# Performance work log

Hardware: AMD Instinct MI355X
Metric: run time of the kernel (lower is better)

Reference implementation:

```python
import jax, jax.numpy as jnp
import numpy as np


def _rpad(x):
    # reflect-pad by 1 on both sides along the last dim (matches torch helper)
    return jnp.concatenate([x[..., 1:2], x, x[..., -2:-1]], axis=-1)


def _fwd1d(x):
    # LeGall 5/3 forward lifting along the last dim
    even = x[..., 0::2]
    odd = x[..., 1::2]
    e = _rpad(even)
    pred = 0.5 * (e[..., :-2] + e[..., 2:])
    d = odd - pred                      # detail
    de = _rpad(d)
    upd = 0.25 * (de[..., :-2] + de[..., 2:])
    s = even + upd                      # approx
    return s, d


def setup_inputs() -> dict:
    key = jax.random.key(0)
    # (B, C, H, W) with even H, W so the odd-size reflect pad branch is inactive
    x = jax.random.normal(key, (8, 3, 1024, 1024), dtype=jnp.float32)
    return {"x": x}


def reference(x):
    # rows: transform along W (last dim)
    s_row, d_row = _fwd1d(x)
    # columns: transform along H by swapping H<->W, lifting, swapping back
    LL, LH = _fwd1d(jnp.swapaxes(s_row, 2, 3))
    HL, HH = _fwd1d(jnp.swapaxes(d_row, 2, 3))
    LL, LH, HL, HH = (jnp.swapaxes(t, 2, 3) for t in (LL, LH, HL, HH))
    # (B, 4C, H/2, W/2) subband order [LL, LH, HL, HH]
    return jnp.concatenate([LL, LH, HL, HH], axis=1)
```

## Files before the change

kernel.cpp:

```cpp
#include <hip/hip_runtime.h>


static __device__ __forceinline__ int mref(int k) {
    return k < 0 ? 1 : (k > 511 ? 510 : k);
}

static __device__ __forceinline__ float4 lift_sub(float4 o, float4 em, float4 ep) {
    float4 r;
    r.x = o.x - 0.5f * (em.x + ep.x);
    r.y = o.y - 0.5f * (em.y + ep.y);
    r.z = o.z - 0.5f * (em.z + ep.z);
    r.w = o.w - 0.5f * (em.w + ep.w);
    return r;
}

static __device__ __forceinline__ float4 lift_add(float4 e, float4 dm, float4 dp) {
    float4 r;
    r.x = e.x + 0.25f * (dm.x + dp.x);
    r.y = e.y + 0.25f * (dm.y + dp.y);
    r.z = e.z + 0.25f * (dm.z + dp.z);
    r.w = e.w + 0.25f * (dm.w + dp.w);
    return r;
}

__global__ __launch_bounds__(256) void ilwt53_v4(const float* __restrict__ x,
                                                 float* __restrict__ out) {
    const int tid = threadIdx.x;
    const int c0  = blockIdx.x * 32;
    const int r0  = blockIdx.y * 32;
    const int img = blockIdx.z;
    const int rb  = 2 * r0 - 4;

    __shared__ float sS[71 * 36];
    __shared__ float sD[71 * 36];

    const float* __restrict__ xim = x + (size_t)img * (1024 * 1024);

    #pragma unroll
    for (int it = 0; it < 2; ++it) {
        int i = tid + it * 256;
        if (i < 284) {
            int lr = i >> 2, g = i & 3;
            int gy = rb + lr; gy = gy < 0 ? 0 : (gy > 1023 ? 1023 : gy);
            const float* __restrict__ row = xim + (size_t)gy * 1024;
            int c  = c0 + 8 * g;
            int fb = 2 * c - 4;

            float w[24];
            if (fb >= 0 && fb + 23 <= 1023) {
                const float4* p = (const float4*)(row + fb);
                #pragma unroll
                for (int q = 0; q < 6; ++q) {
                    float4 v = p[q];
                    w[4*q] = v.x; w[4*q+1] = v.y; w[4*q+2] = v.z; w[4*q+3] = v.w;
                }
            } else {
                #pragma unroll
                for (int q = 0; q < 24; ++q) {
                    int gx = fb + q; gx = gx < 0 ? 0 : (gx > 1023 ? 1023 : gx);
                    w[q] = row[gx];
                }
            }
            float d[10];
            #pragma unroll
            for (int t = 0; t < 10; ++t)
                d[t] = w[2*t+3] - 0.5f * (w[2*t] + w[2*t+4]);
            if (c == 0)   d[1] = w[5]  - w[6];
            if (c == 504) d[8] = w[19] - w[16];

            float s[8];
            #pragma unroll
            for (int i2 = 0; i2 < 8; ++i2)
                s[i2] = w[2*i2+4] + 0.25f * (d[i2] + d[i2+2]);
            if (c == 0)   s[0] = w[4]  + 0.5f * d[2];
            if (c == 504) s[7] = w[18] + 0.5f * d[7];

            float4* ps = (float4*)(sS + lr * 36 + 8 * g);
            ps[0] = make_float4(s[0], s[1], s[2], s[3]);
            ps[1] = make_float4(s[4], s[5], s[6], s[7]);
            float4* pd = (float4*)(sD + lr * 36 + 8 * g);
            pd[0] = make_float4(d[1], d[2], d[3], d[4]);
            pd[1] = make_float4(d[5], d[6], d[7], d[8]);
        }
    }
    __syncthreads();

    {
        const int rr = tid >> 3, ccg = tid & 7;
        const int r  = r0 + rr;
        const int co = 4 * ccg;
        const int k1 = mref(r - 1), k2 = mref(r + 1);
        const int ka = mref(k1 - 1), kb = mref(k1 + 1);
        const int kc = mref(k2 - 1), kd = mref(k2 + 1);

        #define SE_(k) (*(const float4*)(sS + (2 * ((k) - r0) + 4) * 36 + co))
        #define SO_(k) (*(const float4*)(sS + (2 * ((k) - r0) + 5) * 36 + co))
        #define DE_(k) (*(const float4*)(sD + (2 * ((k) - r0) + 4) * 36 + co))
        #define DO_(k) (*(const float4*)(sD + (2 * ((k) - r0) + 5) * 36 + co))

        const size_t plane = 512 * 512;
        float* __restrict__ ob = out + ((size_t)(img / 3) * 12 + (img % 3)) * plane;
        const size_t o = (size_t)r * 512 + c0 + co;

        {
            float4 se_r  = SE_(r);
            float4 se_k1 = SE_(k1);
            float4 se_k2 = SE_(k2);
            float4 se_a  = SE_(ka);
            float4 se_b  = SE_(kb);
            float4 se_c  = SE_(kc);
            float4 se_d  = SE_(kd);
            float4 so_r  = SO_(r);
            float4 so_k1 = SO_(k1);
            float4 so_k2 = SO_(k2);

            float4 lh_c = lift_sub(so_r,  se_k1, se_k2);
            float4 lh_m = lift_sub(so_k1, se_a,  se_b);
            float4 lh_p = lift_sub(so_k2, se_c,  se_d);
            float4 ll   = lift_add(se_r, lh_m, lh_p);

            *(float4*)(ob + o)             = ll;
            *(float4*)(ob + o + 3 * plane) = lh_c;
        }
        {
            float4 de_r  = DE_(r);
            float4 de_k1 = DE_(k1);
            float4 de_k2 = DE_(k2);
            float4 de_a  = DE_(ka);
            float4 de_b  = DE_(kb);
            float4 de_c  = DE_(kc);
            float4 de_d  = DE_(kd);
            float4 do_r  = DO_(r);
            float4 do_k1 = DO_(k1);
            float4 do_k2 = DO_(k2);

            float4 hh_c = lift_sub(do_r,  de_k1, de_k2);
            float4 hh_m = lift_sub(do_k1, de_a,  de_b);
            float4 hh_p = lift_sub(do_k2, de_c,  de_d);
            float4 hl   = lift_add(de_r, hh_m, hh_p);

            *(float4*)(ob + o + 6 * plane) = hl;
            *(float4*)(ob + o + 9 * plane) = hh_c;
        }
        #undef SE_
        #undef SO_
        #undef DE_
        #undef DO_
    }
}

extern "C" void kernel_launch(void* const* d_in, const int* in_sizes, int n_in,
                              void* d_out, int out_size, void* d_ws, size_t ws_size,
                              hipStream_t stream) {
    const float* x = (const float*)d_in[0];
    float* out = (float*)d_out;
    dim3 grid(16, 16, 24);
    dim3 block(256);
    hipLaunchKernelGGL(ilwt53_v4, grid, block, 0, stream, x, out);
}
```

Measured before the change: 178.3 us.

## Drop shared-memory staging and recompute row lifts per thread from global loads

Each thread now performs the horizontal lifting for the eight input rows it needs directly from global memory and computes its output column-lift in registers. The shared-memory tile and the block barrier are removed. The aim is to cut LDS traffic, synchronisation and the halo-staging phase. In exchange, each input row is loaded and lifted by several threads (about 4x redundant loads and ALU work), so the kernel leans on L1/L2 caching to absorb the repeated reads.

```diff
diff --git a/kernel.cpp b/kernel.cpp
--- a/kernel.cpp
+++ b/kernel.cpp
@@ -23,130 +23,86 @@
     return r;
 }
 
-__global__ __launch_bounds__(256) void ilwt53_v4(const float* __restrict__ x,
+static __device__ __forceinline__ void hlift4(const float* __restrict__ row,
+                                              int c, float4* s4, float4* d4) {
+    const int fb = 2 * c - 4;
+    float w[16];
+    if (fb >= 0 && fb + 15 <= 1023) {
+        const float4* p = (const float4*)(row + fb);
+        #pragma unroll
+        for (int q = 0; q < 4; ++q) {
+            float4 v = p[q];
+            w[4*q+0] = v.x; w[4*q+1] = v.y; w[4*q+2] = v.z; w[4*q+3] = v.w;
+        }
+    } else {
+        #pragma unroll
+        for (int t = 0; t < 16; ++t) {
+            int gx = fb + t; gx = gx < 0 ? 0 : (gx > 1023 ? 1023 : gx);
+            w[t] = row[gx];
+        }
+    }
+    float dd[6];
+    #pragma unroll
+    for (int t = 0; t < 6; ++t)
+        dd[t] = w[2*t+3] - 0.5f * (w[2*t] + w[2*t+4]);
+    if (c == 0)   { dd[1] = w[5]  - w[6]; dd[0] = dd[2]; }
+    if (c == 508) { dd[4] = w[11] - w[8]; dd[5] = dd[3]; }
+    float ss[4];
+    #pragma unroll
+    for (int i = 0; i < 4; ++i)
+        ss[i] = w[2*i+4] + 0.25f * (dd[i] + dd[i+2]);
+    *s4 = make_float4(ss[0], ss[1], ss[2], ss[3]);
+    *d4 = make_float4(dd[1], dd[2], dd[3], dd[4]);
+}
+
+__global__ __launch_bounds__(256) void ilwt53_v5(const float* __restrict__ x,
                                                  float* __restrict__ out) {
     const int tid = threadIdx.x;
     const int c0  = blockIdx.x * 32;
     const int r0  = blockIdx.y * 32;
     const int img = blockIdx.z;
-    const int rb  = 2 * r0 - 4;
-
-    __shared__ float sS[71 * 36];
-    __shared__ float sD[71 * 36];
 
     const float* __restrict__ xim = x + (size_t)img * (1024 * 1024);
 
-    #pragma unroll
-    for (int it = 0; it < 2; ++it) {
-        int i = tid + it * 256;
-        if (i < 284) {
-            int lr = i >> 2, g = i & 3;
-            int gy = rb + lr; gy = gy < 0 ? 0 : (gy > 1023 ? 1023 : gy);
-            const float* __restrict__ row = xim + (size_t)gy * 1024;
-            int c  = c0 + 8 * g;
-            int fb = 2 * c - 4;
+    const int rr = tid >> 3, ccg = tid & 7;
+    const int r  = r0 + rr;
+    const int c  = c0 + 4 * ccg;
 
-            float w[24];
-            if (fb >= 0 && fb + 23 <= 1023) {
-                const float4* p = (const float4*)(row + fb);
-                #pragma unroll
-                for (int q = 0; q < 6; ++q) {
-                    float4 v = p[q];
-                    w[4*q] = v.x; w[4*q+1] = v.y; w[4*q+2] = v.z; w[4*q+3] = v.w;
-                }
-            } else {
-                #pragma unroll
-                for (int q = 0; q < 24; ++q) {
-                    int gx = fb + q; gx = gx < 0 ? 0 : (gx > 1023 ? 1023 : gx);
-                    w[q] = row[gx];
-                }
-            }
-            float d[10];
-            #pragma unroll
-            for (int t = 0; t < 10; ++t)
-                d[t] = w[2*t+3] - 0.5f * (w[2*t] + w[2*t+4]);
-            if (c == 0)   d[1] = w[5]  - w[6];
-            if (c == 504) d[8] = w[19] - w[16];
+    const int k1 = mref(r - 1), k2 = mref(r + 1);
+    const int ka = mref(k1 - 1), kd = mref(k2 + 1);
 
-            float s[8];
-            #pragma unroll
-            for (int i2 = 0; i2 < 8; ++i2)
-                s[i2] = w[2*i2+4] + 0.25f * (d[i2] + d[i2+2]);
-            if (c == 0)   s[0] = w[4]  + 0.5f * d[2];
-            if (c == 504) s[7] = w[18] + 0.5f * d[7];
+    float4 se_a, de_a, se_1, de_1, se_r, de_r, se_2, de_2, se_d, de_d;
+    float4 so_1, do_1, so_r, do_r, so_2, do_2;
+    hlift4(xim + (size_t)(2 * ka)     * 1024, c, &se_a, &de_a);
+    hlift4(xim + (size_t)(2 * k1)     * 1024, c, &se_1, &de_1);
+    hlift4(xim + (size_t)(2 * r )     * 1024, c, &se_r, &de_r);
+    hlift4(xim + (size_t)(2 * k2)     * 1024, c, &se_2, &de_2);
+    hlift4(xim + (size_t)(2 * kd)     * 1024, c, &se_d, &de_d);
+    hlift4(xim + (size_t)(2 * k1 + 1) * 1024, c, &so_1, &do_1);
+    hlift4(xim + (size_t)(2 * r  + 1) * 1024, c, &so_r, &do_r);
+    hlift4(xim + (size_t)(2 * k2 + 1) * 1024, c, &so_2, &do_2);
 
-            float4* ps = (float4*)(sS + lr * 36 + 8 * g);
-            ps[0] = make_float4(s[0], s[1], s[2], s[3]);
-            ps[1] = make_float4(s[4], s[5], s[6], s[7]);
-            float4* pd = (float4*)(sD + lr * 36 + 8 * g);
-            pd[0] = make_float4(d[1], d[2], d[3], d[4]);
-            pd[1] = make_float4(d[5], d[6], d[7], d[8]);
-        }
-    }
-    __syncthreads();
+    const float4 seB = (r == 0)   ? se_d : se_r;
+    const float4 seE = (r == 511) ? se_a : se_r;
+    const float4 deB = (r == 0)   ? de_d : de_r;
+    const float4 deE = (r == 511) ? de_a : de_r;
 
-    {
-        const int rr = tid >> 3, ccg = tid & 7;
-        const int r  = r0 + rr;
-        const int co = 4 * ccg;
-        const int k1 = mref(r - 1), k2 = mref(r + 1);
-        const int ka = mref(k1 - 1), kb = mref(k1 + 1);
-        const int kc = mref(k2 - 1), kd = mref(k2 + 1);
+    const float4 lh_m = lift_sub(so_1, se_a, seB);
+    const float4 lh_c = lift_sub(so_r, se_1, se_2);
+    const float4 lh_p = lift_sub(so_2, seE, se_d);
+    const float4 ll   = lift_add(se_r, lh_m, lh_p);
+    const float4 hh_m = lift_sub(do_1, de_a, deB);
+    const float4 hh_c = lift_sub(do_r, de_1, de_2);
+    const float4 hh_p = lift_sub(do_2, deE, de_d);
+    const float4 hl   = lift_add(de_r, hh_m, hh_p);
 
-        #define SE_(k) (*(const float4*)(sS + (2 * ((k) - r0) + 4) * 36 + co))
-        #define SO_(k) (*(const float4*)(sS + (2 * ((k) - r0) + 5) * 36 + co))
-        #define DE_(k) (*(const float4*)(sD + (2 * ((k) - r0) + 4) * 36 + co))
-        #define DO_(k) (*(const float4*)(sD + (2 * ((k) - r0) + 5) * 36 + co))
-
-        const size_t plane = 512 * 512;
-        float* __restrict__ ob = out + ((size_t)(img / 3) * 12 + (img % 3)) * plane;
-        const size_t o = (size_t)r * 512 + c0 + co;
-
-        {
-            float4 se_r  = SE_(r);
-            float4 se_k1 = SE_(k1);
-            float4 se_k2 = SE_(k2);
-            float4 se_a  = SE_(ka);
-            float4 se_b  = SE_(kb);
-            float4 se_c  = SE_(kc);
-            float4 se_d  = SE_(kd);
-            float4 so_r  = SO_(r);
-            float4 so_k1 = SO_(k1);
-            float4 so_k2 = SO_(k2);
-
-            float4 lh_c = lift_sub(so_r,  se_k1, se_k2);
-            float4 lh_m = lift_sub(so_k1, se_a,  se_b);
-            float4 lh_p = lift_sub(so_k2, se_c,  se_d);
-            float4 ll   = lift_add(se_r, lh_m, lh_p);
-
-            *(float4*)(ob + o)             = ll;
-            *(float4*)(ob + o + 3 * plane) = lh_c;
-        }
-        {
-            float4 de_r  = DE_(r);
-            float4 de_k1 = DE_(k1);
-            float4 de_k2 = DE_(k2);
-            float4 de_a  = DE_(ka);
-            float4 de_b  = DE_(kb);
-            float4 de_c  = DE_(kc);
-            float4 de_d  = DE_(kd);
-            float4 do_r  = DO_(r);
-            float4 do_k1 = DO_(k1);
-            float4 do_k2 = DO_(k2);
-
-            float4 hh_c = lift_sub(do_r,  de_k1, de_k2);
-            float4 hh_m = lift_sub(do_k1, de_a,  de_b);
-            float4 hh_p = lift_sub(do_k2, de_c,  de_d);
-            float4 hl   = lift_add(de_r, hh_m, hh_p);
-
-            *(float4*)(ob + o + 6 * plane) = hl;
-            *(float4*)(ob + o + 9 * plane) = hh_c;
-        }
-        #undef SE_
-        #undef SO_
-        #undef DE_
-        #undef DO_
-    }
+    const size_t plane = 512 * 512;
+    float* __restrict__ ob = out + ((size_t)(img / 3) * 12 + (img % 3)) * plane;
+    const size_t o = (size_t)r * 512 + c;
+    *(float4*)(ob + o)             = ll;
+    *(float4*)(ob + o + 3 * plane) = lh_c;
+    *(float4*)(ob + o + 6 * plane) = hl;
+    *(float4*)(ob + o + 9 * plane) = hh_c;
 }
 
 extern "C" void kernel_launch(void* const* d_in, const int* in_sizes, int n_in,
@@ -156,5 +112,5 @@
     float* out = (float*)d_out;
     dim3 grid(16, 16, 24);
     dim3 block(256);
-    hipLaunchKernelGGL(ilwt53_v4, grid, block, 0, stream, x, out);
+    hipLaunchKernelGGL(ilwt53_v5, grid, block, 0, stream, x, out);
 }
```

Result: slower. 209.1 us (+17.3%).

## Stage raw input tile in shared memory with coalesced float4 loads

Applied to the files above, without the earlier changes.

Adds a first phase where all threads cooperatively load the 71x72 raw input halo tile into shared memory using contiguous float4 loads issued in batch. The row-lifting phase then reads its 24-wide windows from LDS instead of doing strided per-thread global loads. The S and D buffers are merged into one interleaved array with an odd float4 row stride to reduce bank conflicts. This costs an extra barrier and more LDS per block, which may lower occupancy.

```diff
diff --git a/kernel.cpp b/kernel.cpp
--- a/kernel.cpp
+++ b/kernel.cpp
@@ -23,7 +23,9 @@
     return r;
 }
 
-__global__ __launch_bounds__(256) void ilwt53_v4(const float* __restrict__ x,
+#define RSTRIDE 19
+
+__global__ __launch_bounds__(256) void ilwt53_v6(const float* __restrict__ x,
                                                  float* __restrict__ out) {
     const int tid = threadIdx.x;
     const int c0  = blockIdx.x * 32;
@@ -31,43 +33,64 @@
     const int img = blockIdx.z;
     const int rb  = 2 * r0 - 4;
 
-    __shared__ float sS[71 * 36];
-    __shared__ float sD[71 * 36];
+    __shared__ float4 raw4[71 * RSTRIDE];
+    __shared__ float4 sd4 [71 * RSTRIDE];
 
     const float* __restrict__ xim = x + (size_t)img * (1024 * 1024);
+
+    {
+        float4 v[5];
+        int    dst[5];
+        bool   act[5];
+        #pragma unroll
+        for (int it = 0; it < 5; ++it) {
+            int idx = tid + it * 256;
+            act[it] = idx < 71 * 18;
+            if (act[it]) {
+                int rw = idx / 18;
+                int q  = idx - rw * 18;
+                dst[it] = rw * RSTRIDE + q;
+                int gy = rb + rw; gy = gy < 0 ? 0 : (gy > 1023 ? 1023 : gy);
+                const float* rp = xim + (size_t)gy * 1024;
+                int fb = 2 * c0 - 4 + 4 * q;
+                if (fb >= 0 && fb + 3 <= 1023) {
+                    v[it] = *(const float4*)(rp + fb);
+                } else {
+                    float a[4];
+                    #pragma unroll
+                    for (int e = 0; e < 4; ++e) {
+                        int gx = fb + e; gx = gx < 0 ? 0 : (gx > 1023 ? 1023 : gx);
+                        a[e] = rp[gx];
+                    }
+                    v[it] = make_float4(a[0], a[1], a[2], a[3]);
+                }
+            }
+        }
+        #pragma unroll
+        for (int it = 0; it < 5; ++it)
+            if (act[it]) raw4[dst[it]] = v[it];
+    }
+    __syncthreads();
 
     #pragma unroll
     for (int it = 0; it < 2; ++it) {
         int i = tid + it * 256;
         if (i < 284) {
             int lr = i >> 2, g = i & 3;
-            int gy = rb + lr; gy = gy < 0 ? 0 : (gy > 1023 ? 1023 : gy);
-            const float* __restrict__ row = xim + (size_t)gy * 1024;
-            int c  = c0 + 8 * g;
-            int fb = 2 * c - 4;
-
+            const float4* wr = raw4 + lr * RSTRIDE + 4 * g;
             float w[24];
-            if (fb >= 0 && fb + 23 <= 1023) {
-                const float4* p = (const float4*)(row + fb);
-                #pragma unroll
-                for (int q = 0; q < 6; ++q) {
-                    float4 v = p[q];
-                    w[4*q] = v.x; w[4*q+1] = v.y; w[4*q+2] = v.z; w[4*q+3] = v.w;
-                }
-            } else {
-                #pragma unroll
-                for (int q = 0; q < 24; ++q) {
-                    int gx = fb + q; gx = gx < 0 ? 0 : (gx > 1023 ? 1023 : gx);
-                    w[q] = row[gx];
-                }
+            #pragma unroll
+            for (int q = 0; q < 6; ++q) {
+                float4 t = wr[q];
+                w[4*q] = t.x; w[4*q+1] = t.y; w[4*q+2] = t.z; w[4*q+3] = t.w;
             }
+            int c = c0 + 8 * g;
             float d[10];
             #pragma unroll
             for (int t = 0; t < 10; ++t)
                 d[t] = w[2*t+3] - 0.5f * (w[2*t] + w[2*t+4]);
             if (c == 0)   d[1] = w[5]  - w[6];
             if (c == 504) d[8] = w[19] - w[16];
-
             float s[8];
             #pragma unroll
             for (int i2 = 0; i2 < 8; ++i2)
@@ -75,10 +98,10 @@
             if (c == 0)   s[0] = w[4]  + 0.5f * d[2];
             if (c == 504) s[7] = w[18] + 0.5f * d[7];
 
-            float4* ps = (float4*)(sS + lr * 36 + 8 * g);
+            float4* ps = sd4 + lr * RSTRIDE + 2 * g;
             ps[0] = make_float4(s[0], s[1], s[2], s[3]);
             ps[1] = make_float4(s[4], s[5], s[6], s[7]);
-            float4* pd = (float4*)(sD + lr * 36 + 8 * g);
+            float4* pd = sd4 + lr * RSTRIDE + 9 + 2 * g;
             pd[0] = make_float4(d[1], d[2], d[3], d[4]);
             pd[1] = make_float4(d[5], d[6], d[7], d[8]);
         }
@@ -88,19 +111,18 @@
     {
         const int rr = tid >> 3, ccg = tid & 7;
         const int r  = r0 + rr;
-        const int co = 4 * ccg;
         const int k1 = mref(r - 1), k2 = mref(r + 1);
         const int ka = mref(k1 - 1), kb = mref(k1 + 1);
         const int kc = mref(k2 - 1), kd = mref(k2 + 1);
 
-        #define SE_(k) (*(const float4*)(sS + (2 * ((k) - r0) + 4) * 36 + co))
-        #define SO_(k) (*(const float4*)(sS + (2 * ((k) - r0) + 5) * 36 + co))
-        #define DE_(k) (*(const float4*)(sD + (2 * ((k) - r0) + 4) * 36 + co))
-        #define DO_(k) (*(const float4*)(sD + (2 * ((k) - r0) + 5) * 36 + co))
+        #define SE_(k) (sd4[(2 * ((k) - r0) + 4) * RSTRIDE + ccg])
+        #define SO_(k) (sd4[(2 * ((k) - r0) + 5) * RSTRIDE + ccg])
+        #define DE_(k) (sd4[(2 * ((k) - r0) + 4) * RSTRIDE + 9 + ccg])
+        #define DO_(k) (sd4[(2 * ((k) - r0) + 5) * RSTRIDE + 9 + ccg])
 
         const size_t plane = 512 * 512;
         float* __restrict__ ob = out + ((size_t)(img / 3) * 12 + (img % 3)) * plane;
-        const size_t o = (size_t)r * 512 + c0 + co;
+        const size_t o = (size_t)r * 512 + c0 + 4 * ccg;
 
         {
             float4 se_r  = SE_(r);
@@ -156,5 +178,5 @@
     float* out = (float*)d_out;
     dim3 grid(16, 16, 24);
     dim3 block(256);
-    hipLaunchKernelGGL(ilwt53_v4, grid, block, 0, stream, x, out);
+    hipLaunchKernelGGL(ilwt53_v6, grid, block, 0, stream, x, out);
 }
```

Measured after the change: 172.7 us. -3.1%, faster.

## Split block tile into per-wave strips to eliminate block barrier

Applied to the files above, without the earlier changes.

Each 64-lane wave now processes its own 8-row output strip with a private shared-memory staging area holding the 24 input rows it needs. This removes the block-wide __syncthreads so waves can proceed independently. In exchange, vertical halo rows are loaded and row-transformed redundantly (96 row-loads per 32 output rows instead of 71), increasing global/L2 traffic and ALU work. It also relies on intra-wave ordering of LDS writes and reads without an explicit barrier.

```diff
diff --git a/kernel.cpp b/kernel.cpp
--- a/kernel.cpp
+++ b/kernel.cpp
@@ -23,23 +23,27 @@
     return r;
 }
 
-__global__ __launch_bounds__(256) void ilwt53_v4(const float* __restrict__ x,
+__global__ __launch_bounds__(256) void ilwt53_v8(const float* __restrict__ x,
                                                  float* __restrict__ out) {
-    const int tid = threadIdx.x;
-    const int c0  = blockIdx.x * 32;
-    const int r0  = blockIdx.y * 32;
-    const int img = blockIdx.z;
-    const int rb  = 2 * r0 - 4;
+    const int tid  = threadIdx.x;
+    const int lane = tid & 63;
+    const int wv   = tid >> 6;
+    const int c0   = blockIdx.x * 32;
+    const int R0   = blockIdx.y * 32 + wv * 8;
+    const int img  = blockIdx.z;
+    const int rb   = 2 * R0 - 4;
 
-    __shared__ float sS[71 * 36];
-    __shared__ float sD[71 * 36];
+    __shared__ float sS[4][24 * 36];
+    __shared__ float sD[4][24 * 36];
+    float* __restrict__ wS = sS[wv];
+    float* __restrict__ wD = sD[wv];
 
     const float* __restrict__ xim = x + (size_t)img * (1024 * 1024);
 
     #pragma unroll
     for (int it = 0; it < 2; ++it) {
-        int i = tid + it * 256;
-        if (i < 284) {
+        int i = lane + it * 64;
+        if (i < 96) {
             int lr = i >> 2, g = i & 3;
             int gy = rb + lr; gy = gy < 0 ? 0 : (gy > 1023 ? 1023 : gy);
             const float* __restrict__ row = xim + (size_t)gy * 1024;
@@ -67,7 +71,6 @@
                 d[t] = w[2*t+3] - 0.5f * (w[2*t] + w[2*t+4]);
             if (c == 0)   d[1] = w[5]  - w[6];
             if (c == 504) d[8] = w[19] - w[16];
-
             float s[8];
             #pragma unroll
             for (int i2 = 0; i2 < 8; ++i2)
@@ -75,28 +78,27 @@
             if (c == 0)   s[0] = w[4]  + 0.5f * d[2];
             if (c == 504) s[7] = w[18] + 0.5f * d[7];
 
-            float4* ps = (float4*)(sS + lr * 36 + 8 * g);
+            float4* ps = (float4*)(wS + lr * 36 + 8 * g);
             ps[0] = make_float4(s[0], s[1], s[2], s[3]);
             ps[1] = make_float4(s[4], s[5], s[6], s[7]);
-            float4* pd = (float4*)(sD + lr * 36 + 8 * g);
+            float4* pd = (float4*)(wD + lr * 36 + 8 * g);
             pd[0] = make_float4(d[1], d[2], d[3], d[4]);
             pd[1] = make_float4(d[5], d[6], d[7], d[8]);
         }
     }
-    __syncthreads();
 
     {
-        const int rr = tid >> 3, ccg = tid & 7;
-        const int r  = r0 + rr;
-        const int co = 4 * ccg;
+        const int rr = lane >> 3, ccg = lane & 7;
+        const int r  = R0 + rr;
         const int k1 = mref(r - 1), k2 = mref(r + 1);
         const int ka = mref(k1 - 1), kb = mref(k1 + 1);
         const int kc = mref(k2 - 1), kd = mref(k2 + 1);
+        const int co = 4 * ccg;
 
-        #define SE_(k) (*(const float4*)(sS + (2 * ((k) - r0) + 4) * 36 + co))
-        #define SO_(k) (*(const float4*)(sS + (2 * ((k) - r0) + 5) * 36 + co))
-        #define DE_(k) (*(const float4*)(sD + (2 * ((k) - r0) + 4) * 36 + co))
-        #define DO_(k) (*(const float4*)(sD + (2 * ((k) - r0) + 5) * 36 + co))
+        #define SE_(k) (*(const float4*)(wS + (2 * ((k) - R0) + 4) * 36 + co))
+        #define SO_(k) (*(const float4*)(wS + (2 * ((k) - R0) + 5) * 36 + co))
+        #define DE_(k) (*(const float4*)(wD + (2 * ((k) - R0) + 4) * 36 + co))
+        #define DO_(k) (*(const float4*)(wD + (2 * ((k) - R0) + 5) * 36 + co))
 
         const size_t plane = 512 * 512;
         float* __restrict__ ob = out + ((size_t)(img / 3) * 12 + (img % 3)) * plane;
@@ -156,5 +158,5 @@
     float* out = (float*)d_out;
     dim3 grid(16, 16, 24);
     dim3 block(256);
-    hipLaunchKernelGGL(ilwt53_v4, grid, block, 0, stream, x, out);
+    hipLaunchKernelGGL(ilwt53_v8, grid, block, 0, stream, x, out);
 }
```

Result: slower. 184.7 us (+3.6%).
